# Kernel optimization log

Measured on AMD Instinct MI355X. Metric: run time of the kernel, lower is better.

## Reference

```python
import jax, jax.numpy as jnp
import numpy as np

# -------- configuration (production-scale segmentation head) --------
BS, C, H, W = 8, 256, 96, 96
N = H * W          # nodes in the spanning tree (flattened pixels)
E = N - 1          # spanning-tree edge count
ZETA_G = 0.01      # default zeta_g of Global_APro.forward


def setup_inputs() -> dict:
    key = jax.random.key(0)
    k1, k2 = jax.random.split(key)
    feature_in = jax.random.normal(k1, (BS, 1, H, W), dtype=jnp.float32)
    # scaled so norm2 distances over C=256 channels stay O(1..10)
    embed_in = 0.1 * jax.random.normal(k2, (BS, C, H, W), dtype=jnp.float32)
    # Random spanning trees, one per batch element. Edges are topologically
    # ordered: edge e connects parent=src[e] < child=tgt[e]=e+1, so processing
    # edges in order is a valid root->leaf sweep (and reversed is leaf->root).
    rng = np.random.default_rng(0)
    trees = []
    children = np.arange(1, N, dtype=np.int32)
    for _ in range(BS):
        parents = np.floor(rng.random(E) * np.arange(1, N)).astype(np.int32)
        trees.append(np.stack([parents, children], axis=1))
    tree = jnp.asarray(np.stack(trees, axis=0))  # [BS, E, 2] int32
    return {"feature_in": feature_in, "embed_in": embed_in, "tree": tree}


def _gp_single(f, wgt, src, tgt):
    """Global affinity propagation (tree filter) on one tree.
    Computes out_i = sum_j A_ij f_j / sum_j A_ij with A_ij = prod of edge
    affinities along the unique tree path i->j, via the classic two-pass DP.
    f: [N], wgt/src/tgt: [E] (edges topologically ordered, parent=src).
    """
    ones = jnp.ones_like(f)

    def up(carry, xs):                 # leaf -> root aggregation
        S, Z = carry
        s, t, we = xs
        S = S.at[s].add(we * S[t])
        Z = Z.at[s].add(we * Z[t])
        return (S, Z), None

    (S, Z), _ = jax.lax.scan(up, (f, ones), (src, tgt, wgt), reverse=True)

    def down(carry, xs):               # root -> leaf propagation
        F, G = carry
        s, t, we = xs
        F = F.at[t].set(we * F[s] + (1.0 - we * we) * F[t])
        G = G.at[t].set(we * G[s] + (1.0 - we * we) * G[t])
        return (F, G), None

    (F, G), _ = jax.lax.scan(down, (S, Z), (src, tgt, wgt))
    return F / G


def reference(feature_in, embed_in, tree):
    bs, c, h, w = embed_in.shape
    n = h * w
    emb = embed_in.reshape(bs, c, n)               # [bs, c, N]
    src = tree[:, :, 0]                            # [bs, E]
    tgt = tree[:, :, 1]                            # [bs, E]
    # gather node embeddings along tree edges (get_true_index)
    gather = jax.vmap(lambda e, i: e[:, i])        # [c, N], [E] -> [c, E]
    src_node = gather(emb, src)                    # [bs, c, E]
    tgt_node = gather(emb, tgt)                    # [bs, c, E]
    diff = src_node - tgt_node
    dist = jnp.sum(diff * diff, axis=1)            # norm2_distance -> [bs, E]
    wgt = jnp.exp(-ZETA_G * dist)                  # edge affinity
    f = feature_in.reshape(bs, n)                  # [bs, N]
    out = jax.vmap(_gp_single)(f, wgt, src, tgt)   # [bs, N]
    return out.reshape(bs, 1, h, w)
```

## Files before the change

kernel.cpp:

```cpp
#include <hip/hip_runtime.h>
#include <hip/hip_bf16.h>
#include <hip/hip_fp16.h>

#define BS 8
#define C  256
#define N  9216
#define E  9215
#define MAXD 128
#define LVL_STRIDE 192

__global__ __launch_bounds__(256) void transpose_kernel(const float* __restrict__ emb,
                                                        __half* __restrict__ embT) {
    const int b  = blockIdx.z;
    const int c0 = blockIdx.y * 64;
    const int n0 = blockIdx.x * 64;
    __shared__ __half tile[64][65];

    const int nn = threadIdx.x & 63;
    const int cg = threadIdx.x >> 6;
    const float* src = emb + ((size_t)b * C + c0) * N + n0;
    #pragma unroll
    for (int k = 0; k < 16; ++k) {
        int cc = cg * 16 + k;
        tile[cc][nn] = __float2half(src[(size_t)cc * N + nn]);
    }
    __syncthreads();

    const int cp = threadIdx.x & 31;
    const int ng = threadIdx.x >> 5;
    __half* dst = embT + ((size_t)b * N + n0) * C + c0;
    #pragma unroll
    for (int k = 0; k < 8; ++k) {
        int n2 = ng * 8 + k;
        __half2 v = __halves2half2(tile[2 * cp][n2], tile[2 * cp + 1][n2]);
        *(__half2*)(dst + (size_t)n2 * C + 2 * cp) = v;
    }
}

__global__ __launch_bounds__(256) void weights_kernel(const __half* __restrict__ embT,
                                                      const int* __restrict__ tree,
                                                      float* __restrict__ wgt) {
    const int b   = blockIdx.y;
    const int tid = threadIdx.x;
    const int lane = tid & 63;
    const int wid  = tid >> 6;
    const int sub  = lane >> 5;
    const int l    = lane & 31;
    const int e    = (blockIdx.x * 4 + wid) * 2 + sub;

    float acc = 0.f;
    if (e < E) {
        int s = tree[(b * E + e) * 2];
        int t = tree[(b * E + e) * 2 + 1];
        const float4* ps = (const float4*)(embT + ((size_t)b * N + s) * C) + l;
        const float4* pt = (const float4*)(embT + ((size_t)b * N + t) * C) + l;
        float4 av = *ps;
        float4 bv = *pt;
        const __half2* ah = (const __half2*)&av;
        const __half2* bh = (const __half2*)&bv;
        #pragma unroll
        for (int j = 0; j < 4; ++j) {
            float2 fa = __half22float2(ah[j]);
            float2 fb = __half22float2(bh[j]);
            float d0 = fa.x - fb.x;
            float d1 = fa.y - fb.y;
            acc += d0 * d0 + d1 * d1;
        }
    }
    #pragma unroll
    for (int m = 16; m >= 1; m >>= 1) acc += __shfl_xor(acc, m);
    if (l == 0 && e < E) wgt[b * N + e] = __expf(-0.01f * acc);
}

__global__ __launch_bounds__(1024) void levels_kernel(const int* __restrict__ tree,
                                                      const float* __restrict__ wgt,
                                                      int2* __restrict__ tsw,
                                                      int* __restrict__ lvlOff) {
    const int b = blockIdx.x;
    const int tid = threadIdx.x;
    __shared__ int P[N];
    __shared__ int cnt[MAXD];
    __shared__ int off[MAXD + 1];

    const int* tb = tree + b * E * 2;

    for (int t = tid; t < N; t += 1024) {
        P[t] = (t == 0) ? 0 : (tb[(t - 1) * 2] | (1 << 16));
    }
    for (int i = tid; i < MAXD; i += 1024) cnt[i] = 0;
    __syncthreads();

    for (int it = 0; it < 6; ++it) {
        int np[9];
        int k = 0;
        for (int t = tid; t < N; t += 1024, ++k) {
            int p = P[t];
            int pa = P[p & 0xffff];
            np[k] = (pa & 0xffff) | ((p >> 16) + (pa >> 16)) << 16;
        }
        __syncthreads();
        k = 0;
        for (int t = tid; t < N; t += 1024, ++k) P[t] = np[k];
        __syncthreads();
    }

    for (int t = 1 + tid; t < N; t += 1024) {
        int d = P[t] >> 16; if (d > MAXD - 1) d = MAXD - 1;
        atomicAdd(&cnt[d], 1);
    }
    __syncthreads();
    if (tid == 0) {
        int acc = 0, mx = 1;
        for (int d = 0; d < MAXD; ++d) {
            off[d] = acc; acc += cnt[d];
            if (cnt[d] > 0) mx = d;
        }
        off[MAXD] = acc;
        lvlOff[b * LVL_STRIDE + MAXD + 1] = mx;
    }
    __syncthreads();
    for (int i = tid; i < MAXD; i += 1024) cnt[i] = 0;
    __syncthreads();

    for (int t = 1 + tid; t < N; t += 1024) {
        int d = P[t] >> 16; if (d > MAXD - 1) d = MAXD - 1;
        int pos = off[d] + atomicAdd(&cnt[d], 1);
        int p = tb[(t - 1) * 2];
        tsw[b * N + pos] = make_int2(t | (p << 16),
                                     __float_as_int(wgt[b * N + t - 1]));
    }
    for (int i = tid; i <= MAXD; i += 1024) lvlOff[b * LVL_STRIDE + i] = off[i];
}

__global__ __launch_bounds__(1024) void dp_kernel(const float* __restrict__ feat,
                                                  const int* __restrict__ lvlOff,
                                                  const int2* __restrict__ tsw,
                                                  float* __restrict__ out) {
    const int b = blockIdx.x;
    const int tid = threadIdx.x;
    __shared__ float2 V[N];
    __shared__ int off[MAXD + 1];
    __shared__ int maxd_s;

    for (int i = tid; i <= MAXD; i += 1024) off[i] = lvlOff[b * LVL_STRIDE + i];
    if (tid == 0) maxd_s = lvlOff[b * LVL_STRIDE + MAXD + 1];
    for (int i = tid; i < N; i += 1024) V[i] = make_float2(feat[b * N + i], 1.0f);
    __syncthreads();
    const int maxd = maxd_s;
    const int2* tw = tsw + b * N;

    for (int lev = maxd; lev >= 1; --lev) {
        int s0 = off[lev], s1 = off[lev + 1];
        for (int i = s0 + tid; i < s1; i += 1024) {
            int2 ew = tw[i];
            int t = ew.x & 0xffff, s = ew.x >> 16;
            float w = __int_as_float(ew.y);
            float2 vt = V[t];
            atomicAdd(&V[s].x, w * vt.x);
            atomicAdd(&V[s].y, w * vt.y);
        }
        __syncthreads();
    }
    for (int lev = 1; lev <= maxd; ++lev) {
        int s0 = off[lev], s1 = off[lev + 1];
        for (int i = s0 + tid; i < s1; i += 1024) {
            int2 ew = tw[i];
            int t = ew.x & 0xffff, s = ew.x >> 16;
            float w = __int_as_float(ew.y);
            float2 vs = V[s], vt = V[t];
            float c = 1.f - w * w;
            V[t] = make_float2(w * vs.x + c * vt.x, w * vs.y + c * vt.y);
        }
        __syncthreads();
    }
    for (int i = tid; i < N; i += 1024) {
        float2 v = V[i];
        out[b * N + i] = v.x / v.y;
    }
}

extern "C" void kernel_launch(void* const* d_in, const int* in_sizes, int n_in,
                              void* d_out, int out_size, void* d_ws, size_t ws_size,
                              hipStream_t stream) {
    const float* feat = (const float*)d_in[0];
    const float* emb  = (const float*)d_in[1];
    const int*   tree = (const int*)d_in[2];
    float* out = (float*)d_out;

    const size_t BN = (size_t)BS * N;
    float* wgt    = (float*)d_ws;
    int2*  tsw    = (int2*)((char*)d_ws + BN * 4);
    int*   lvlOff = (int*)((char*)d_ws + BN * 12);
    __half* embT  = (__half*)((char*)d_ws +
                     ((BN * 12 + BS * LVL_STRIDE * 4 + 255) / 256) * 256);

    transpose_kernel<<<dim3(N / 64, C / 64, BS), 256, 0, stream>>>(emb, embT);
    weights_kernel<<<dim3((E + 7) / 8, BS), 256, 0, stream>>>(embT, tree, wgt);
    levels_kernel<<<BS, 1024, 0, stream>>>(tree, wgt, tsw, lvlOff);
    dp_kernel<<<BS, 1024, 0, stream>>>(feat, lvlOff, tsw, out);
}
```

Measured before the change: 189.4 us.

## Fuse level ordering into transpose launch and fetch weights by node in DP

```diff
diff --git a/kernel.cpp b/kernel.cpp
--- a/kernel.cpp
+++ b/kernel.cpp
@@ -8,32 +8,91 @@
 #define E  9215
 #define MAXD 128
 #define LVL_STRIDE 192
-
-__global__ __launch_bounds__(256) void transpose_kernel(const float* __restrict__ emb,
-                                                        __half* __restrict__ embT) {
-    const int b  = blockIdx.z;
-    const int c0 = blockIdx.y * 64;
-    const int n0 = blockIdx.x * 64;
-    __shared__ __half tile[64][65];
-
-    const int nn = threadIdx.x & 63;
-    const int cg = threadIdx.x >> 6;
-    const float* src = emb + ((size_t)b * C + c0) * N + n0;
-    #pragma unroll
-    for (int k = 0; k < 16; ++k) {
-        int cc = cg * 16 + k;
-        tile[cc][nn] = __float2half(src[(size_t)cc * N + nn]);
-    }
-    __syncthreads();
-
-    const int cp = threadIdx.x & 31;
-    const int ng = threadIdx.x >> 5;
-    __half* dst = embT + ((size_t)b * N + n0) * C + c0;
-    #pragma unroll
-    for (int k = 0; k < 8; ++k) {
-        int n2 = ng * 8 + k;
-        __half2 v = __halves2half2(tile[2 * cp][n2], tile[2 * cp + 1][n2]);
-        *(__half2*)(dst + (size_t)n2 * C + 2 * cp) = v;
+#define TSLABS (N / 64)
+
+__global__ __launch_bounds__(1024) void setup_kernel(const float* __restrict__ emb,
+                                                     __half* __restrict__ embT,
+                                                     const int* __restrict__ tree,
+                                                     int* __restrict__ tsArr,
+                                                     int* __restrict__ lvlOff) {
+    __shared__ int P[N];
+    __shared__ int cnt[MAXD];
+    __shared__ int off[MAXD + 1];
+    const int tid = threadIdx.x;
+
+    if (blockIdx.x < BS) {
+        const int b = blockIdx.x;
+        const int* tb = tree + b * E * 2;
+
+        for (int t = tid; t < N; t += 1024)
+            P[t] = (t == 0) ? 0 : (tb[(t - 1) * 2] | (1 << 16));
+        for (int i = tid; i < MAXD; i += 1024) cnt[i] = 0;
+        __syncthreads();
+
+        for (int it = 0; it < 6; ++it) {
+            int np[9];
+            int k = 0;
+            for (int t = tid; t < N; t += 1024, ++k) {
+                int p = P[t];
+                int pa = P[p & 0xffff];
+                np[k] = (pa & 0xffff) | ((p >> 16) + (pa >> 16)) << 16;
+            }
+            __syncthreads();
+            k = 0;
+            for (int t = tid; t < N; t += 1024, ++k) P[t] = np[k];
+            __syncthreads();
+        }
+
+        for (int t = 1 + tid; t < N; t += 1024) {
+            int d = P[t] >> 16; if (d > MAXD - 1) d = MAXD - 1;
+            atomicAdd(&cnt[d], 1);
+        }
+        __syncthreads();
+        if (tid == 0) {
+            int acc = 0, mx = 1;
+            for (int d = 0; d < MAXD; ++d) {
+                off[d] = acc; acc += cnt[d];
+                if (cnt[d] > 0) mx = d;
+            }
+            off[MAXD] = acc;
+            lvlOff[b * LVL_STRIDE + MAXD + 1] = mx;
+        }
+        __syncthreads();
+        for (int i = tid; i < MAXD; i += 1024) cnt[i] = 0;
+        __syncthreads();
+
+        for (int t = 1 + tid; t < N; t += 1024) {
+            int d = P[t] >> 16; if (d > MAXD - 1) d = MAXD - 1;
+            int pos = off[d] + atomicAdd(&cnt[d], 1);
+            int p = tb[(t - 1) * 2];
+            tsArr[b * N + pos] = t | (p << 16);
+        }
+        for (int i = tid; i <= MAXD; i += 1024) lvlOff[b * LVL_STRIDE + i] = off[i];
+    } else {
+        const int tb = blockIdx.x - BS;
+        const int b  = tb & 7;
+        const int n0 = (tb >> 3) * 64;
+        __half (*tile)[65] = (__half(*)[65])P;
+
+        const int nn = tid & 63;
+        const int cg = tid >> 6;
+        const float* src = emb + (size_t)b * C * N + n0;
+        #pragma unroll
+        for (int k = 0; k < 16; ++k) {
+            int cc = cg * 16 + k;
+            tile[cc][nn] = __float2half(src[(size_t)cc * N + nn]);
+        }
+        __syncthreads();
+
+        const int cp = tid & 127;
+        const int ng = tid >> 7;
+        __half* dst = embT + ((size_t)b * N + n0) * C;
+        #pragma unroll
+        for (int k = 0; k < 8; ++k) {
+            int n2 = ng * 8 + k;
+            __half2 v = __halves2half2(tile[2 * cp][n2], tile[2 * cp + 1][n2]);
+            *(__half2*)(dst + (size_t)n2 * C + 2 * cp) = v;
+        }
     }
 }
 
@@ -72,69 +131,10 @@
     if (l == 0 && e < E) wgt[b * N + e] = __expf(-0.01f * acc);
 }
 
-__global__ __launch_bounds__(1024) void levels_kernel(const int* __restrict__ tree,
-                                                      const float* __restrict__ wgt,
-                                                      int2* __restrict__ tsw,
-                                                      int* __restrict__ lvlOff) {
-    const int b = blockIdx.x;
-    const int tid = threadIdx.x;
-    __shared__ int P[N];
-    __shared__ int cnt[MAXD];
-    __shared__ int off[MAXD + 1];
-
-    const int* tb = tree + b * E * 2;
-
-    for (int t = tid; t < N; t += 1024) {
-        P[t] = (t == 0) ? 0 : (tb[(t - 1) * 2] | (1 << 16));
-    }
-    for (int i = tid; i < MAXD; i += 1024) cnt[i] = 0;
-    __syncthreads();
-
-    for (int it = 0; it < 6; ++it) {
-        int np[9];
-        int k = 0;
-        for (int t = tid; t < N; t += 1024, ++k) {
-            int p = P[t];
-            int pa = P[p & 0xffff];
-            np[k] = (pa & 0xffff) | ((p >> 16) + (pa >> 16)) << 16;
-        }
-        __syncthreads();
-        k = 0;
-        for (int t = tid; t < N; t += 1024, ++k) P[t] = np[k];
-        __syncthreads();
-    }
-
-    for (int t = 1 + tid; t < N; t += 1024) {
-        int d = P[t] >> 16; if (d > MAXD - 1) d = MAXD - 1;
-        atomicAdd(&cnt[d], 1);
-    }
-    __syncthreads();
-    if (tid == 0) {
-        int acc = 0, mx = 1;
-        for (int d = 0; d < MAXD; ++d) {
-            off[d] = acc; acc += cnt[d];
-            if (cnt[d] > 0) mx = d;
-        }
-        off[MAXD] = acc;
-        lvlOff[b * LVL_STRIDE + MAXD + 1] = mx;
-    }
-    __syncthreads();
-    for (int i = tid; i < MAXD; i += 1024) cnt[i] = 0;
-    __syncthreads();
-
-    for (int t = 1 + tid; t < N; t += 1024) {
-        int d = P[t] >> 16; if (d > MAXD - 1) d = MAXD - 1;
-        int pos = off[d] + atomicAdd(&cnt[d], 1);
-        int p = tb[(t - 1) * 2];
-        tsw[b * N + pos] = make_int2(t | (p << 16),
-                                     __float_as_int(wgt[b * N + t - 1]));
-    }
-    for (int i = tid; i <= MAXD; i += 1024) lvlOff[b * LVL_STRIDE + i] = off[i];
-}
-
 __global__ __launch_bounds__(1024) void dp_kernel(const float* __restrict__ feat,
                                                   const int* __restrict__ lvlOff,
-                                                  const int2* __restrict__ tsw,
+                                                  const int* __restrict__ tsArr,
+                                                  const float* __restrict__ wgt,
                                                   float* __restrict__ out) {
     const int b = blockIdx.x;
     const int tid = threadIdx.x;
@@ -147,14 +147,15 @@
     for (int i = tid; i < N; i += 1024) V[i] = make_float2(feat[b * N + i], 1.0f);
     __syncthreads();
     const int maxd = maxd_s;
-    const int2* tw = tsw + b * N;
+    const int* tsA = tsArr + b * N;
+    const float* wG = wgt + b * N;
 
     for (int lev = maxd; lev >= 1; --lev) {
         int s0 = off[lev], s1 = off[lev + 1];
         for (int i = s0 + tid; i < s1; i += 1024) {
-            int2 ew = tw[i];
-            int t = ew.x & 0xffff, s = ew.x >> 16;
-            float w = __int_as_float(ew.y);
+            int ts = tsA[i];
+            int t = ts & 0xffff, s = ts >> 16;
+            float w = wG[t - 1];
             float2 vt = V[t];
             atomicAdd(&V[s].x, w * vt.x);
             atomicAdd(&V[s].y, w * vt.y);
@@ -164,9 +165,9 @@
     for (int lev = 1; lev <= maxd; ++lev) {
         int s0 = off[lev], s1 = off[lev + 1];
         for (int i = s0 + tid; i < s1; i += 1024) {
-            int2 ew = tw[i];
-            int t = ew.x & 0xffff, s = ew.x >> 16;
-            float w = __int_as_float(ew.y);
+            int ts = tsA[i];
+            int t = ts & 0xffff, s = ts >> 16;
+            float w = wG[t - 1];
             float2 vs = V[s], vt = V[t];
             float c = 1.f - w * w;
             V[t] = make_float2(w * vs.x + c * vt.x, w * vs.y + c * vt.y);
@@ -189,13 +190,12 @@
 
     const size_t BN = (size_t)BS * N;
     float* wgt    = (float*)d_ws;
-    int2*  tsw    = (int2*)((char*)d_ws + BN * 4);
-    int*   lvlOff = (int*)((char*)d_ws + BN * 12);
+    int*   tsArr  = (int*)((char*)d_ws + BN * 4);
+    int*   lvlOff = (int*)((char*)d_ws + BN * 8);
     __half* embT  = (__half*)((char*)d_ws +
-                     ((BN * 12 + BS * LVL_STRIDE * 4 + 255) / 256) * 256);
-
-    transpose_kernel<<<dim3(N / 64, C / 64, BS), 256, 0, stream>>>(emb, embT);
+                     ((BN * 8 + BS * LVL_STRIDE * 4 + 255) / 256) * 256);
+
+    setup_kernel<<<BS + TSLABS * BS, 1024, 0, stream>>>(emb, embT, tree, tsArr, lvlOff);
     weights_kernel<<<dim3((E + 7) / 8, BS), 256, 0, stream>>>(embT, tree, wgt);
-    levels_kernel<<<BS, 1024, 0, stream>>>(tree, wgt, tsw, lvlOff);
-    dp_kernel<<<BS, 1024, 0, stream>>>(feat, lvlOff, tsw, out);
-}
+    dp_kernel<<<BS, 1024, 0, stream>>>(feat, lvlOff, tsArr, wgt, out);
+}
```

Result: faster. 179.6 us (-5.1%).
